# Optimization experiments

Hardware: AMD Instinct MI355X
Metric: run time of the kernel (lower is better)

## Reference

```python
import jax, jax.numpy as jnp
import numpy as np

NUM_FEATURES = 20480
NUM_ACCUMULATORS = 128


def setup_inputs() -> dict:
    key = jax.random.key(0)
    k1, k2, k3, k4, k5, k6 = jax.random.split(key, 6)
    B = 4096
    white = jax.random.uniform(k1, (B, NUM_FEATURES), dtype=jnp.float32)
    black = jax.random.uniform(k2, (B, NUM_FEATURES), dtype=jnp.float32)
    # learned params (torch nn.Linear stores weight as [out, in])
    w_psqt = jax.random.normal(k3, (2, NUM_FEATURES), dtype=jnp.float32) * 0.01
    w_acc = jax.random.normal(k4, (NUM_ACCUMULATORS, NUM_FEATURES), dtype=jnp.float32) * 0.01
    b_acc = jax.random.normal(k5, (NUM_ACCUMULATORS,), dtype=jnp.float32) * 0.01
    w_layer = jax.random.normal(k6, (2, NUM_ACCUMULATORS), dtype=jnp.float32) * 0.1
    return {"white": white, "black": black, "w_psqt": w_psqt,
            "w_acc": w_acc, "b_acc": b_acc, "w_layer": w_layer}


def reference(white, black, w_psqt, w_acc, b_acc, w_layer):
    # psqt: Linear(NUM_FEATURES -> 2, no bias)
    psqt = jnp.einsum('bf,of->bo', white, w_psqt) - jnp.einsum('bf,of->bo', black, w_psqt)
    # accumulator: Linear(NUM_FEATURES -> 128) + CReLU clamp(0, 1)
    white_acc = jnp.clip(jnp.einsum('bf,af->ba', white, w_acc) + b_acc, 0.0, 1.0)
    black_acc = jnp.clip(jnp.einsum('bf,af->ba', black, w_acc) + b_acc, 0.0, 1.0)
    # output layer: Linear(128 -> 2, no bias)
    positional = jnp.einsum('ba,oa->bo', white_acc, w_layer) - jnp.einsum('ba,oa->bo', black_acc, w_layer)
    return psqt + positional
```

## Files before the change

### kernel.cpp

```cpp
#include <hip/hip_runtime.h>
#include <hip/hip_bf16.h>
#include <stdint.h>

typedef __attribute__((ext_vector_type(4))) float          f32x4;
typedef __attribute__((ext_vector_type(8))) short          short8;
typedef __attribute__((ext_vector_type(4))) unsigned short u16x4;

#define F            20480
#define NROWS        4096
#define NPAD         144
#define BK           64
#define CHUNK_BYTES  (NPAD * BK * 2)
#define TOTAL_CHUNKS (F / BK)
#define MB           256

static __device__ __forceinline__ unsigned short f2bf(float f) {
    unsigned u = __builtin_bit_cast(unsigned, f);
    unsigned r = (u + 0x7FFFu + ((u >> 16) & 1u)) >> 16;
    return (unsigned short)r;
}

__global__ __launch_bounds__(256) void prep_b(const float* __restrict__ w_acc,
                                              const float* __restrict__ w_psqt,
                                              unsigned short* __restrict__ Bp) {
    int gid = blockIdx.x * 256 + threadIdx.x;
    int p8    = gid * 8;
    int chunk = p8 / CHUNK_BYTES;
    int win   = p8 % CHUNK_BYTES;
    int n     = win >> 7;
    int sb    = win & 127;
    int kbyte = sb ^ ((n & 7) << 4);
    int k0    = chunk * 64 + (kbyte >> 1);
    f32x4 v = {0.f, 0.f, 0.f, 0.f};
    if (n < 128)      v = *(const f32x4*)(w_acc  + (size_t)n * F + k0);
    else if (n < 130) v = *(const f32x4*)(w_psqt + (size_t)(n - 128) * F + k0);
    u16x4 pk;
    pk[0] = f2bf(v[0]); pk[1] = f2bf(v[1]); pk[2] = f2bf(v[2]); pk[3] = f2bf(v[3]);
    *(u16x4*)((char*)Bp + p8) = pk;
}

__global__ __launch_bounds__(512, 2) void gemm_main(
    const float* __restrict__ white, const float* __restrict__ black,
    const unsigned short* __restrict__ Bp, float* __restrict__ partial,
    int chunks_per_ks)
{
    __shared__ alignas(16) unsigned short Blds[2][CHUNK_BYTES / 2];

    const int tid  = threadIdx.x;
    const int wave = tid >> 6;
    const int lane = tid & 63;
    const int g    = lane >> 4;
    const int r16  = lane & 15;

    const int rg   = blockIdx.x;
    const int row0 = rg * MB;
    const float* Aside = (row0 < NROWS) ? white : black;
    const int arow0 = row0 & (NROWS - 1);

    const int chunk0 = blockIdx.y * chunks_per_ks;
    const int nch    = chunks_per_ks;

    const float* aRow0 = Aside + (size_t)(arow0 + wave * 32 + r16) * F + g * 8;
    const float* aRow1 = aRow0 + (size_t)16 * F;

    f32x4 apf[2][2][2];
    f32x4 acc[2][9];
    const f32x4 zero = {0.f, 0.f, 0.f, 0.f};
    #pragma unroll
    for (int m = 0; m < 2; ++m)
        #pragma unroll
        for (int n = 0; n < 9; ++n) acc[m][n] = zero;

    auto stageB = [&](int buf, int chunk) {
        const char* src = (const char*)Bp + (size_t)chunk * CHUNK_BYTES + lane * 16;
        char* dst = (char*)(&Blds[buf][0]);
        #pragma unroll
        for (int line = 0; line < 3; ++line) {
            int li = wave + line * 8;
            if (li < 18)
                __builtin_amdgcn_global_load_lds(
                    (const __attribute__((address_space(1))) void*)(src + li * 1024),
                    (__attribute__((address_space(3))) void*)(dst + li * 1024),
                    16, 0, 0);
        }
    };

    auto loadA = [&](int kbase) {
        const float* p0 = aRow0 + kbase;
        const float* p1 = aRow1 + kbase;
        apf[0][0][0] = *(const f32x4*)(p0);
        apf[0][0][1] = *(const f32x4*)(p0 + 4);
        apf[0][1][0] = *(const f32x4*)(p0 + 32);
        apf[0][1][1] = *(const f32x4*)(p0 + 36);
        apf[1][0][0] = *(const f32x4*)(p1);
        apf[1][0][1] = *(const f32x4*)(p1 + 4);
        apf[1][1][0] = *(const f32x4*)(p1 + 32);
        apf[1][1][1] = *(const f32x4*)(p1 + 36);
    };

    stageB(0, chunk0);
    loadA(chunk0 * BK);

    for (int t = 0; t < nch; ++t) {
        __syncthreads();

        short8 afr[2][2];
        #pragma unroll
        for (int m = 0; m < 2; ++m)
            #pragma unroll
            for (int kk = 0; kk < 2; ++kk) {
                short8 r;
                #pragma unroll
                for (int j = 0; j < 4; ++j) {
                    r[j]     = (short)f2bf(apf[m][kk][0][j]);
                    r[j + 4] = (short)f2bf(apf[m][kk][1][j]);
                }
                afr[m][kk] = r;
            }

        if (t + 1 < nch) {
            stageB((t + 1) & 1, chunk0 + t + 1);
            loadA((chunk0 + t + 1) * BK);
        }

        const char* bb = (const char*)(&Blds[t & 1][0]);
        #pragma unroll
        for (int kk = 0; kk < 2; ++kk) {
            #pragma unroll
            for (int n = 0; n < 9; ++n) {
                const int nn  = n * 16 + r16;
                const int off = nn * 128 + ((kk * 64 + g * 16) ^ ((nn & 7) << 4));
                short8 bf = *(const short8*)(bb + off);
                acc[0][n] = __builtin_amdgcn_mfma_f32_16x16x32_bf16(afr[0][kk], bf, acc[0][n], 0, 0, 0);
                acc[1][n] = __builtin_amdgcn_mfma_f32_16x16x32_bf16(afr[1][kk], bf, acc[1][n], 0, 0, 0);
            }
        }
    }

    float* prow = partial + ((size_t)blockIdx.y * 8192 + row0 + wave * 32 + g * 4) * NPAD;
    #pragma unroll
    for (int m = 0; m < 2; ++m)
        #pragma unroll
        for (int n = 0; n < 9; ++n)
            #pragma unroll
            for (int j = 0; j < 4; ++j)
                prow[(m * 16 + j) * NPAD + n * 16 + r16] = acc[m][n][j];
}

__global__ __launch_bounds__(256) void epilogue(
    const float* __restrict__ partial, const float* __restrict__ b_acc,
    const float* __restrict__ w_layer, float* __restrict__ out, int KS)
{
    const int wave = threadIdx.x >> 6, lane = threadIdx.x & 63;
    const int b = blockIdx.x * 4 + wave;
    float sw0 = 0, sw1 = 0, sb0 = 0, sb1 = 0, q0 = 0, q1 = 0;
    for (int ks = 0; ks < KS; ++ks) {
        const float* Pw = partial + ((size_t)ks * 8192 + b) * NPAD;
        const float* Pb = partial + ((size_t)ks * 8192 + NROWS + b) * NPAD;
        sw0 += Pw[lane];      sw1 += Pw[lane + 64];
        sb0 += Pb[lane];      sb1 += Pb[lane + 64];
        q0  += Pw[128] - Pb[128];
        q1  += Pw[129] - Pb[129];
    }
    float wa0 = fminf(fmaxf(sw0 + b_acc[lane], 0.f), 1.f);
    float wa1 = fminf(fmaxf(sw1 + b_acc[lane + 64], 0.f), 1.f);
    float ba0 = fminf(fmaxf(sb0 + b_acc[lane], 0.f), 1.f);
    float ba1 = fminf(fmaxf(sb1 + b_acc[lane + 64], 0.f), 1.f);
    float d0 = wa0 - ba0, d1 = wa1 - ba1;
    float p0 = w_layer[lane] * d0       + w_layer[lane + 64] * d1;
    float p1 = w_layer[128 + lane] * d0 + w_layer[192 + lane] * d1;
    #pragma unroll
    for (int off = 32; off >= 1; off >>= 1) {
        p0 += __shfl_xor(p0, off, 64);
        p1 += __shfl_xor(p1, off, 64);
    }
    if (lane == 0) {
        out[b * 2 + 0] = q0 + p0;
        out[b * 2 + 1] = q1 + p1;
    }
}

extern "C" void kernel_launch(void* const* d_in, const int* in_sizes, int n_in,
                              void* d_out, int out_size, void* d_ws, size_t ws_size,
                              hipStream_t stream)
{
    const float* white   = (const float*)d_in[0];
    const float* black   = (const float*)d_in[1];
    const float* w_psqt  = (const float*)d_in[2];
    const float* w_acc   = (const float*)d_in[3];
    const float* b_acc   = (const float*)d_in[4];
    const float* w_layer = (const float*)d_in[5];
    float* out = (float*)d_out;

    const size_t bbytes = (size_t)TOTAL_CHUNKS * CHUNK_BYTES;
    unsigned short* Bp = (unsigned short*)d_ws;
    float* partial = (float*)((char*)d_ws + bbytes);

    const size_t per_ks = (size_t)8192 * NPAD * 4;
    int KS = 1;
    const int cands[5] = {8, 5, 4, 2, 1};
    for (int i = 0; i < 5; ++i)
        if (bbytes + (size_t)cands[i] * per_ks <= ws_size) { KS = cands[i]; break; }
    int chunks_per_ks = TOTAL_CHUNKS / KS;

    prep_b   <<<dim3(2880),   dim3(256), 0, stream>>>(w_acc, w_psqt, Bp);
    gemm_main<<<dim3(32, KS), dim3(512), 0, stream>>>(white, black, Bp, partial, chunks_per_ks);
    epilogue <<<dim3(1024),   dim3(256), 0, stream>>>(partial, b_acc, w_layer, out, KS);
}
```

Baseline: 162.7 us.

## Double K-chunk to 128 and store split-K partials as fp16

```diff
diff --git a/kernel.cpp b/kernel.cpp
--- a/kernel.cpp
+++ b/kernel.cpp
@@ -9,7 +9,7 @@
 #define F            20480
 #define NROWS        4096
 #define NPAD         144
-#define BK           64
+#define BK           128
 #define CHUNK_BYTES  (NPAD * BK * 2)
 #define TOTAL_CHUNKS (F / BK)
 #define MB           256
@@ -27,10 +27,10 @@
     int p8    = gid * 8;
     int chunk = p8 / CHUNK_BYTES;
     int win   = p8 % CHUNK_BYTES;
-    int n     = win >> 7;
-    int sb    = win & 127;
+    int n     = win >> 8;
+    int sb    = win & 255;
     int kbyte = sb ^ ((n & 7) << 4);
-    int k0    = chunk * 64 + (kbyte >> 1);
+    int k0    = chunk * BK + (kbyte >> 1);
     f32x4 v = {0.f, 0.f, 0.f, 0.f};
     if (n < 128)      v = *(const f32x4*)(w_acc  + (size_t)n * F + k0);
     else if (n < 130) v = *(const f32x4*)(w_psqt + (size_t)(n - 128) * F + k0);
@@ -41,7 +41,7 @@
 
 __global__ __launch_bounds__(512, 2) void gemm_main(
     const float* __restrict__ white, const float* __restrict__ black,
-    const unsigned short* __restrict__ Bp, float* __restrict__ partial,
+    const unsigned short* __restrict__ Bp, _Float16* __restrict__ partial,
     int chunks_per_ks)
 {
     __shared__ alignas(16) unsigned short Blds[2][CHUNK_BYTES / 2];
@@ -63,7 +63,7 @@
     const float* aRow0 = Aside + (size_t)(arow0 + wave * 32 + r16) * F + g * 8;
     const float* aRow1 = aRow0 + (size_t)16 * F;
 
-    f32x4 apf[2][2][2];
+    f32x4 apf[2][4][2];
     f32x4 acc[2][9];
     const f32x4 zero = {0.f, 0.f, 0.f, 0.f};
     #pragma unroll
@@ -75,9 +75,9 @@
         const char* src = (const char*)Bp + (size_t)chunk * CHUNK_BYTES + lane * 16;
         char* dst = (char*)(&Blds[buf][0]);
         #pragma unroll
-        for (int line = 0; line < 3; ++line) {
+        for (int line = 0; line < 5; ++line) {
             int li = wave + line * 8;
-            if (li < 18)
+            if (li < 36)
                 __builtin_amdgcn_global_load_lds(
                     (const __attribute__((address_space(1))) void*)(src + li * 1024),
                     (__attribute__((address_space(3))) void*)(dst + li * 1024),
@@ -86,16 +86,15 @@
     };
 
     auto loadA = [&](int kbase) {
-        const float* p0 = aRow0 + kbase;
-        const float* p1 = aRow1 + kbase;
-        apf[0][0][0] = *(const f32x4*)(p0);
-        apf[0][0][1] = *(const f32x4*)(p0 + 4);
-        apf[0][1][0] = *(const f32x4*)(p0 + 32);
-        apf[0][1][1] = *(const f32x4*)(p0 + 36);
-        apf[1][0][0] = *(const f32x4*)(p1);
-        apf[1][0][1] = *(const f32x4*)(p1 + 4);
-        apf[1][1][0] = *(const f32x4*)(p1 + 32);
-        apf[1][1][1] = *(const f32x4*)(p1 + 36);
+        #pragma unroll
+        for (int m = 0; m < 2; ++m) {
+            const float* p = (m ? aRow1 : aRow0) + kbase;
+            #pragma unroll
+            for (int kk = 0; kk < 4; ++kk) {
+                apf[m][kk][0] = *(const f32x4*)(p + kk * 32);
+                apf[m][kk][1] = *(const f32x4*)(p + kk * 32 + 4);
+            }
+        }
     };
 
     stageB(0, chunk0);
@@ -104,11 +103,11 @@
     for (int t = 0; t < nch; ++t) {
         __syncthreads();
 
-        short8 afr[2][2];
+        short8 afr[2][4];
         #pragma unroll
         for (int m = 0; m < 2; ++m)
             #pragma unroll
-            for (int kk = 0; kk < 2; ++kk) {
+            for (int kk = 0; kk < 4; ++kk) {
                 short8 r;
                 #pragma unroll
                 for (int j = 0; j < 4; ++j) {
@@ -125,11 +124,11 @@
 
         const char* bb = (const char*)(&Blds[t & 1][0]);
         #pragma unroll
-        for (int kk = 0; kk < 2; ++kk) {
+        for (int kk = 0; kk < 4; ++kk) {
             #pragma unroll
             for (int n = 0; n < 9; ++n) {
                 const int nn  = n * 16 + r16;
-                const int off = nn * 128 + ((kk * 64 + g * 16) ^ ((nn & 7) << 4));
+                const int off = nn * 256 + ((kk * 64 + g * 16) ^ ((nn & 7) << 4));
                 short8 bf = *(const short8*)(bb + off);
                 acc[0][n] = __builtin_amdgcn_mfma_f32_16x16x32_bf16(afr[0][kk], bf, acc[0][n], 0, 0, 0);
                 acc[1][n] = __builtin_amdgcn_mfma_f32_16x16x32_bf16(afr[1][kk], bf, acc[1][n], 0, 0, 0);
@@ -137,30 +136,30 @@
         }
     }
 
-    float* prow = partial + ((size_t)blockIdx.y * 8192 + row0 + wave * 32 + g * 4) * NPAD;
+    _Float16* prow = partial + ((size_t)blockIdx.y * 8192 + row0 + wave * 32 + g * 4) * NPAD;
     #pragma unroll
     for (int m = 0; m < 2; ++m)
         #pragma unroll
         for (int n = 0; n < 9; ++n)
             #pragma unroll
             for (int j = 0; j < 4; ++j)
-                prow[(m * 16 + j) * NPAD + n * 16 + r16] = acc[m][n][j];
+                prow[(m * 16 + j) * NPAD + n * 16 + r16] = (_Float16)acc[m][n][j];
 }
 
 __global__ __launch_bounds__(256) void epilogue(
-    const float* __restrict__ partial, const float* __restrict__ b_acc,
+    const _Float16* __restrict__ partial, const float* __restrict__ b_acc,
     const float* __restrict__ w_layer, float* __restrict__ out, int KS)
 {
     const int wave = threadIdx.x >> 6, lane = threadIdx.x & 63;
     const int b = blockIdx.x * 4 + wave;
     float sw0 = 0, sw1 = 0, sb0 = 0, sb1 = 0, q0 = 0, q1 = 0;
     for (int ks = 0; ks < KS; ++ks) {
-        const float* Pw = partial + ((size_t)ks * 8192 + b) * NPAD;
-        const float* Pb = partial + ((size_t)ks * 8192 + NROWS + b) * NPAD;
-        sw0 += Pw[lane];      sw1 += Pw[lane + 64];
-        sb0 += Pb[lane];      sb1 += Pb[lane + 64];
-        q0  += Pw[128] - Pb[128];
-        q1  += Pw[129] - Pb[129];
+        const _Float16* Pw = partial + ((size_t)ks * 8192 + b) * NPAD;
+        const _Float16* Pb = partial + ((size_t)ks * 8192 + NROWS + b) * NPAD;
+        sw0 += (float)Pw[lane];      sw1 += (float)Pw[lane + 64];
+        sb0 += (float)Pb[lane];      sb1 += (float)Pb[lane + 64];
+        q0  += (float)Pw[128] - (float)Pb[128];
+        q1  += (float)Pw[129] - (float)Pb[129];
     }
     float wa0 = fminf(fmaxf(sw0 + b_acc[lane], 0.f), 1.f);
     float wa1 = fminf(fmaxf(sw1 + b_acc[lane + 64], 0.f), 1.f);
@@ -194,9 +193,9 @@
 
     const size_t bbytes = (size_t)TOTAL_CHUNKS * CHUNK_BYTES;
     unsigned short* Bp = (unsigned short*)d_ws;
-    float* partial = (float*)((char*)d_ws + bbytes);
-
-    const size_t per_ks = (size_t)8192 * NPAD * 4;
+    _Float16* partial = (_Float16*)((char*)d_ws + bbytes);
+
+    const size_t per_ks = (size_t)8192 * NPAD * 2;
     int KS = 1;
     const int cands[5] = {8, 5, 4, 2, 1};
     for (int i = 0; i < 5; ++i)
```

Measured after the change: 149.1 us. 1.09x faster.
